# Kernel optimization log

Hardware: AMD Instinct MI355X
Metric: run time of the kernel (lower is better)

The kernel has to match this reference:

```python
import jax, jax.numpy as jnp
import numpy as np
import math

INPUT_SIZE = 1024
B, L1, L2 = 8, 2048, 2048


def setup_inputs() -> dict:
    key = jax.random.key(0)
    ks = jax.random.split(key, 10)
    s = 1.0 / math.sqrt(INPUT_SIZE)
    return {
        "Q": jax.random.normal(ks[0], (B, L1, INPUT_SIZE), dtype=jnp.float32),
        "K": jax.random.normal(ks[1], (B, L2, INPUT_SIZE), dtype=jnp.float32),
        "V": jax.random.normal(ks[2], (B, L2, INPUT_SIZE), dtype=jnp.float32),
        "K_mask": jax.random.randint(ks[3], (B, L2), 0, 2, dtype=jnp.int32),
        "Wq": jax.random.normal(ks[4], (INPUT_SIZE, INPUT_SIZE), dtype=jnp.float32) * s,
        "bq": jax.random.normal(ks[5], (INPUT_SIZE,), dtype=jnp.float32) * s,
        "Wk": jax.random.normal(ks[6], (INPUT_SIZE, INPUT_SIZE), dtype=jnp.float32) * s,
        "bk": jax.random.normal(ks[7], (INPUT_SIZE,), dtype=jnp.float32) * s,
        "Wv": jax.random.normal(ks[8], (INPUT_SIZE, INPUT_SIZE), dtype=jnp.float32) * s,
        "bv": jax.random.normal(ks[9], (INPUT_SIZE,), dtype=jnp.float32) * s,
    }


def reference(Q, K, V, K_mask, Wq, bq, Wk, bk, Wv, bv):
    # Linear projections (torch Linear: x @ W.T + b)
    q = jnp.einsum('bld,ed->ble', Q, Wq) + bq
    k = jnp.einsum('bld,ed->ble', K, Wk) + bk
    v = jnp.einsum('bld,ed->ble', V, Wv) + bv
    # scores: [B, L1, L2], scaled by sqrt(input_size)
    scores = jnp.einsum('bqd,bkd->bqk', q, k) / math.sqrt(INPUT_SIZE)
    # K_mask == 1 marks padding -> -inf before softmax
    scores = jnp.where(K_mask[:, None, :] == 1, -jnp.inf, scores)
    alpha = jax.nn.softmax(scores, axis=-1)
    matched_seq = jnp.einsum('bqk,bkd->bqd', alpha, v)
    return matched_seq
```

## Files before the change

### kernel.cpp

```cpp
#include <hip/hip_runtime.h>


using u16 = unsigned short;
using frag_ab = __attribute__((ext_vector_type(8))) short;
using frag_cd = __attribute__((ext_vector_type(4))) float;

#define BAR() asm volatile("s_barrier" ::: "memory")
#define WAITV(n) asm volatile("s_waitcnt vmcnt(" #n ")" ::: "memory")
#define WAITLGKM0() do { asm volatile("s_waitcnt lgkmcnt(0)" ::: "memory"); \
                         __builtin_amdgcn_sched_barrier(0); } while (0)
#define L(d, ab, h) (lds + (((d) * 4) + ((ab) * 2) + (h)) * 8192)

__device__ __forceinline__ u16 f2bf(float f) {
  union { float f; unsigned u; } c; c.f = f;
  unsigned u = c.u;
  return (u16)((u + 0x7FFFu + ((u >> 16) & 1u)) >> 16);
}
__device__ __forceinline__ u16 f2h(float f) {
  union { _Float16 h; u16 u; } c; c.h = (_Float16)f; return c.u;
}
__device__ __forceinline__ float h2f(u16 u) {
  union { u16 u; _Float16 h; } c; c.u = u; return (float)c.h;
}

__device__ __forceinline__ void async_ld16(const void* g, void* l) {
  __builtin_amdgcn_global_load_lds(
      (const __attribute__((address_space(1))) unsigned*)g,
      (__attribute__((address_space(3))) unsigned*)l, 16, 0, 0);
}

__global__ void cvtw3(const float* __restrict__ a, const float* __restrict__ b,
                      const float* __restrict__ c, u16* __restrict__ out) {
  const float* in = blockIdx.z == 0 ? a : (blockIdx.z == 1 ? b : c);
  u16* o = out + (long)blockIdx.z * 1048576L;
  long i = ((long)blockIdx.x * 256 + threadIdx.x) * 4;
  float4 v = *reinterpret_cast<const float4*>(in + i);
  *reinterpret_cast<ushort4*>(o + i) =
      make_ushort4(f2bf(v.x), f2bf(v.y), f2bf(v.z), f2bf(v.w));
}

__global__ void cvt3_f32_bf16(const float* __restrict__ q, const float* __restrict__ k,
                              const float* __restrict__ v, u16* __restrict__ out) {
  const float* in = blockIdx.z == 0 ? q : (blockIdx.z == 1 ? k : v);
  u16* o = out + (long)blockIdx.z * 16777216L;
  long i = ((long)blockIdx.x * 256 + threadIdx.x) * 4;
  float4 x = *reinterpret_cast<const float4*>(in + i);
  *reinterpret_cast<ushort4*>(o + i) =
      make_ushort4(f2bf(x.x), f2bf(x.y), f2bf(x.z), f2bf(x.w));
}

__device__ __forceinline__ void stage_half(const u16* __restrict__ g_rowbase,
                                           long Kstr, u16* l_half,
                                           int wave, int lane) {
  const int t = wave * 64 + lane;
  #pragma unroll
  for (int i = 0; i < 2; i++) {
    const int row = i * 64 + (t >> 3);
    const int cb  = (t & 7) * 16;
    const int cbs = cb ^ ((row & 7) << 4);
    async_ld16(g_rowbase + (long)row * Kstr + (cbs >> 1),
               l_half + i * 4096 + wave * 512);
  }
}

__device__ __forceinline__ frag_ab ld_frag(const u16* half_base, int r, int k) {
  const int idx = r * 64 + (k ^ ((r & 7) << 3));
  return *reinterpret_cast<const frag_ab*>(half_base + idx);
}

template<int OUT_MODE>
__device__ __forceinline__ void
gemm256_body(const u16* __restrict__ A, const u16* __restrict__ Bt,
             void* __restrict__ Cout, const float* __restrict__ bias,
             int M, int N, int K, long sA, long sB, long sC, float scale,
             u16* lds)
{
  const int gx = gridDim.x, gy = gridDim.y, gz = gridDim.z;
  const int nwg = gx * gy * gz;
  const int lin = ((int)blockIdx.z * gy + blockIdx.y) * gx + blockIdx.x;
  const int q8 = nwg >> 3, r8 = nwg & 7;
  const int xcd = lin & 7, idx8 = lin >> 3;
  const int swz = (xcd < r8 ? xcd * (q8 + 1) : r8 * (q8 + 1) + (xcd - r8) * q8) + idx8;
  const int z = swz / (gx * gy);
  const int rem = swz % (gx * gy);
  const int m0 = (rem / gx) * 256;
  const int n0 = (rem % gx) * 256;

  const u16* Ab = A + (long)z * sA;
  const u16* Bb = Bt + (long)z * sB;

  const int tid = threadIdx.x;
  const int wave = tid >> 6, lane = tid & 63;
  const int wm = wave >> 2, wn = wave & 3;
  const int ln15 = lane & 15, kof = (lane >> 4) * 8;
  const int rB0 = (wn & 1) * 64;
  const int NT = K >> 6;

  frag_cd acc[8][4];
  #pragma unroll
  for (int i = 0; i < 8; i++)
    #pragma unroll
    for (int j = 0; j < 4; j++)
      acc[i][j] = (frag_cd){0.f, 0.f, 0.f, 0.f};

  stage_half(Ab + (long)(m0 +   0) * K, K, L(0, 0, 0), wave, lane);
  stage_half(Ab + (long)(m0 + 128) * K, K, L(0, 0, 1), wave, lane);
  stage_half(Bb + (long)(n0 +   0) * K, K, L(0, 1, 0), wave, lane);
  stage_half(Bb + (long)(n0 + 128) * K, K, L(0, 1, 1), wave, lane);
  {
    const int t1 = (1 < NT) ? 1 : 0;
    stage_half(Bb + (long)(n0 +   0) * K + t1 * 64, K, L(1, 1, 0), wave, lane);
    stage_half(Bb + (long)(n0 + 128) * K + t1 * 64, K, L(1, 1, 1), wave, lane);
  }
  WAITV(4);
  BAR();

  for (int t = 0; t < NT; ++t) {
    const int d = t & 1;
    const u16* Al = L(d, 0, wm);
    const u16* Bl = L(d, 1, wn >> 1);
    const int tA = (t + 1 < NT) ? t + 1 : NT - 1;
    const int tB = (t + 2 < NT) ? t + 2 : NT - 1;

    frag_ab bf[4][2], af[2][2];

    #pragma unroll
    for (int bn = 0; bn < 4; ++bn)
      #pragma unroll
      for (int kk = 0; kk < 2; ++kk)
        bf[bn][kk] = ld_frag(Bl, rB0 + bn * 16 + ln15, kk * 32 + kof);
    #pragma unroll
    for (int am = 0; am < 2; ++am)
      #pragma unroll
      for (int kk = 0; kk < 2; ++kk)
        af[am][kk] = ld_frag(Al, am * 16 + ln15, kk * 32 + kof);
    stage_half(Ab + (long)(m0 +   0) * K + tA * 64, K, L(d ^ 1, 0, 0), wave, lane);
    stage_half(Ab + (long)(m0 + 128) * K + tA * 64, K, L(d ^ 1, 0, 1), wave, lane);
    BAR();
    __builtin_amdgcn_s_setprio(1);
    #pragma unroll
    for (int am = 0; am < 2; ++am)
      #pragma unroll
      for (int bn = 0; bn < 4; ++bn)
        #pragma unroll
        for (int kk = 0; kk < 2; ++kk)
          acc[am][bn] = __builtin_amdgcn_mfma_f32_16x16x32_bf16(af[am][kk], bf[bn][kk], acc[am][bn], 0, 0, 0);
    __builtin_amdgcn_s_setprio(0);
    BAR();

    #pragma unroll
    for (int am = 0; am < 2; ++am)
      #pragma unroll
      for (int kk = 0; kk < 2; ++kk)
        af[am][kk] = ld_frag(Al, (2 + am) * 16 + ln15, kk * 32 + kof);
    stage_half(Bb + (long)(n0 + 0) * K + tB * 64, K, L(d, 1, 0), wave, lane);
    BAR();
    __builtin_amdgcn_s_setprio(1);
    #pragma unroll
    for (int am = 0; am < 2; ++am)
      #pragma unroll
      for (int bn = 0; bn < 4; ++bn)
        #pragma unroll
        for (int kk = 0; kk < 2; ++kk)
          acc[2 + am][bn] = __builtin_amdgcn_mfma_f32_16x16x32_bf16(af[am][kk], bf[bn][kk], acc[2 + am][bn], 0, 0, 0);
    __builtin_amdgcn_s_setprio(0);
    BAR();

    #pragma unroll
    for (int am = 0; am < 2; ++am)
      #pragma unroll
      for (int kk = 0; kk < 2; ++kk)
        af[am][kk] = ld_frag(Al, (4 + am) * 16 + ln15, kk * 32 + kof);
    stage_half(Bb + (long)(n0 + 128) * K + tB * 64, K, L(d, 1, 1), wave, lane);
    BAR();
    __builtin_amdgcn_s_setprio(1);
    #pragma unroll
    for (int am = 0; am < 2; ++am)
      #pragma unroll
      for (int bn = 0; bn < 4; ++bn)
        #pragma unroll
        for (int kk = 0; kk < 2; ++kk)
          acc[4 + am][bn] = __builtin_amdgcn_mfma_f32_16x16x32_bf16(af[am][kk], bf[bn][kk], acc[4 + am][bn], 0, 0, 0);
    __builtin_amdgcn_s_setprio(0);
    BAR();

    #pragma unroll
    for (int am = 0; am < 2; ++am)
      #pragma unroll
      for (int kk = 0; kk < 2; ++kk)
        af[am][kk] = ld_frag(Al, (6 + am) * 16 + ln15, kk * 32 + kof);
    BAR();
    __builtin_amdgcn_s_setprio(1);
    #pragma unroll
    for (int am = 0; am < 2; ++am)
      #pragma unroll
      for (int bn = 0; bn < 4; ++bn)
        #pragma unroll
        for (int kk = 0; kk < 2; ++kk)
          acc[6 + am][bn] = __builtin_amdgcn_mfma_f32_16x16x32_bf16(af[am][kk], bf[bn][kk], acc[6 + am][bn], 0, 0, 0);
    __builtin_amdgcn_s_setprio(0);
    WAITV(4);
    BAR();
  }

  WAITV(0);
  BAR();

  const int cl = lane & 15;
  const int rb = (lane >> 4) * 4;

  if (OUT_MODE == 1 || OUT_MODE == 3) {
    u16* Wt = lds + wave * 8192;
    #pragma unroll
    for (int am = 0; am < 8; ++am)
      #pragma unroll
      for (int bn = 0; bn < 4; ++bn) {
        const int col = bn * 16 + cl;
        const float badd = bias ? bias[n0 + wn * 64 + col] : 0.f;
        #pragma unroll
        for (int r = 0; r < 4; ++r) {
          const int row = am * 16 + rb + r;
          const int slot = (col >> 3) ^ ((row >> 2) & 7);
          const float val = acc[am][bn][r] * scale + badd;
          Wt[row * 64 + slot * 8 + (col & 7)] = (OUT_MODE == 1) ? f2bf(val) : f2h(val);
        }
      }
    WAITLGKM0();
    u16* Cb = (u16*)Cout + (long)z * sC;
    #pragma unroll
    for (int i = 0; i < 16; ++i) {
      const int row = (lane >> 3) + i * 8;
      const int c = lane & 7;
      const int slot = c ^ ((row >> 2) & 7);
      frag_ab v = *reinterpret_cast<const frag_ab*>(Wt + row * 64 + slot * 8);
      const long grow = m0 + wm * 128 + row;
      const int gcol = n0 + wn * 64 + c * 8;
      *reinterpret_cast<frag_ab*>(Cb + grow * N + gcol) = v;
    }
  } else if (OUT_MODE == 0) {
    float* Wt = (float*)(void*)lds + wave * 4096;
    float* Cb = (float*)Cout + (long)z * sC;
    #pragma unroll
    for (int p = 0; p < 2; ++p) {
      #pragma unroll
      for (int am = 0; am < 8; ++am)
        #pragma unroll
        for (int bn = 0; bn < 2; ++bn) {
          const int col = bn * 16 + cl;
          #pragma unroll
          for (int r = 0; r < 4; ++r) {
            const int row = am * 16 + rb + r;
            const int slot = (col >> 2) ^ ((row >> 2) & 7);
            Wt[row * 32 + slot * 4 + (col & 3)] = acc[am][2 * p + bn][r] * scale;
          }
        }
      WAITLGKM0();
      #pragma unroll
      for (int i = 0; i < 16; ++i) {
        const int row = (lane >> 3) + i * 8;
        const int c = lane & 7;
        const int slot = c ^ ((row >> 2) & 7);
        float4 v = *reinterpret_cast<const float4*>(Wt + row * 32 + slot * 4);
        const long grow = m0 + wm * 128 + row;
        const int gcol = n0 + wn * 64 + p * 32 + c * 4;
        *reinterpret_cast<float4*>(Cb + grow * N + gcol) = v;
      }
      if (p == 0) WAITLGKM0();
    }
  } else {
    #pragma unroll
    for (int bn = 0; bn < 4; ++bn) {
      const int gcol = n0 + wn * 64 + bn * 16 + cl;
      const float badd = bias ? bias[gcol] : 0.f;
      #pragma unroll
      for (int am = 0; am < 8; ++am) {
        const int grow0 = m0 + wm * 128 + am * 16 + rb;
        ushort4 pk;
        pk.x = f2bf(acc[am][bn][0] * scale + badd);
        pk.y = f2bf(acc[am][bn][1] * scale + badd);
        pk.z = f2bf(acc[am][bn][2] * scale + badd);
        pk.w = f2bf(acc[am][bn][3] * scale + badd);
        const int bb = grow0 >> 11, l2 = grow0 & 2047;
        *reinterpret_cast<ushort4*>((u16*)Cout + ((long)bb * N + gcol) * 2048L + l2) = pk;
      }
    }
  }
}

__global__ void __launch_bounds__(512, 2)
proj_gemm(const u16* A, const u16* Bt, void* C, const float* bias,
          int M, int N, int K, long sA, long sB, long sC, float scale) {
  __shared__ u16 lds[8 * 8192];
  gemm256_body<1>(A, Bt, C, bias, M, N, K, sA, sB, sC, scale, lds);
}
__global__ void __launch_bounds__(512, 2)
projv_gemm(const u16* A, const u16* Bt, void* C, const float* bias,
           int M, int N, int K, long sA, long sB, long sC, float scale) {
  __shared__ u16 lds[8 * 8192];
  gemm256_body<2>(A, Bt, C, bias, M, N, K, sA, sB, sC, scale, lds);
}
__global__ void __launch_bounds__(512, 2)
qk_gemm(const u16* A, const u16* Bt, void* C, const float* bias,
        int M, int N, int K, long sA, long sB, long sC, float scale) {
  __shared__ u16 lds[8 * 8192];
  gemm256_body<3>(A, Bt, C, bias, M, N, K, sA, sB, sC, scale, lds);
}
__global__ void __launch_bounds__(512, 2)
pv_gemm(const u16* A, const u16* Bt, void* C, const float* bias,
        int M, int N, int K, long sA, long sB, long sC, float scale) {
  __shared__ u16 lds[8 * 8192];
  gemm256_body<0>(A, Bt, C, bias, M, N, K, sA, sB, sC, scale, lds);
}

__global__ void softmax_rows_h(const u16* __restrict__ S, const int* __restrict__ Km,
                               u16* __restrict__ P)
{
  const long row = blockIdx.x;
  const int b = (int)(row >> 11);
  const u16* s = S + row * 2048;
  const int* mask = Km + (long)b * 2048;
  u16* p = P + row * 2048;

  const int t = threadIdx.x;
  const int base = t * 8;

  ushort4 r0 = *reinterpret_cast<const ushort4*>(s + base);
  ushort4 r1 = *reinterpret_cast<const ushort4*>(s + base + 4);
  int4 mA = *reinterpret_cast<const int4*>(mask + base);
  int4 mB = *reinterpret_cast<const int4*>(mask + base + 4);

  float vals[8] = {h2f(r0.x), h2f(r0.y), h2f(r0.z), h2f(r0.w),
                   h2f(r1.x), h2f(r1.y), h2f(r1.z), h2f(r1.w)};
  const int mk[8] = {mA.x, mA.y, mA.z, mA.w, mB.x, mB.y, mB.z, mB.w};

  float mx = -3.0e38f;
  #pragma unroll
  for (int i = 0; i < 8; i++) if (!mk[i]) mx = fmaxf(mx, vals[i]);
  #pragma unroll
  for (int off = 32; off > 0; off >>= 1) mx = fmaxf(mx, __shfl_xor(mx, off));

  __shared__ float redm[4], reds[4];
  const int wave = t >> 6, lane = t & 63;
  if (lane == 0) redm[wave] = mx;
  __syncthreads();
  mx = fmaxf(fmaxf(redm[0], redm[1]), fmaxf(redm[2], redm[3]));

  float e[8]; float sum = 0.f;
  #pragma unroll
  for (int i = 0; i < 8; i++) { e[i] = mk[i] ? 0.f : __expf(vals[i] - mx); sum += e[i]; }
  #pragma unroll
  for (int off = 32; off > 0; off >>= 1) sum += __shfl_xor(sum, off);
  if (lane == 0) reds[wave] = sum;
  __syncthreads();
  sum = reds[0] + reds[1] + reds[2] + reds[3];
  const float inv = 1.f / sum;

  *reinterpret_cast<ushort4*>(p + base) =
      make_ushort4(f2bf(e[0]*inv), f2bf(e[1]*inv), f2bf(e[2]*inv), f2bf(e[3]*inv));
  *reinterpret_cast<ushort4*>(p + base + 4) =
      make_ushort4(f2bf(e[4]*inv), f2bf(e[5]*inv), f2bf(e[6]*inv), f2bf(e[7]*inv));
}

extern "C" void kernel_launch(void* const* d_in, const int* in_sizes, int n_in,
                              void* d_out, int out_size, void* d_ws, size_t ws_size,
                              hipStream_t stream) {
  (void)in_sizes; (void)n_in; (void)out_size;

  const float* Qin  = (const float*)d_in[0];
  const float* Kin  = (const float*)d_in[1];
  const float* Vin  = (const float*)d_in[2];
  const int*   Kmask = (const int*)d_in[3];
  const float* Wq = (const float*)d_in[4];
  const float* bq = (const float*)d_in[5];
  const float* Wk = (const float*)d_in[6];
  const float* bk = (const float*)d_in[7];
  const float* Wv = (const float*)d_in[8];
  const float* bv = (const float*)d_in[9];

  char* ws = (char*)d_ws;
  const size_t MB = 1024UL * 1024UL;
  const dim3 blk(256);
  const dim3 gblk(512);
  const float rs = 0.03125f;

  if (ws_size >= 226 * MB) {
    u16*  qb = (u16*)(ws);
    u16*  kb = (u16*)(ws + 32 * MB);
    u16*  vT = (u16*)(ws + 64 * MB);
    u16*  P  = (u16*)(ws + 96 * MB);
    u16*  Xq = (u16*)(ws + 96 * MB);
    u16*  S  = (u16*)(ws + 160 * MB);
    u16*  Wb = (u16*)(ws + 224 * MB);

    cvt3_f32_bf16<<<dim3(16384, 1, 3), blk, 0, stream>>>(Qin, Kin, Vin, Xq);
    cvtw3<<<dim3(1024, 1, 3), blk, 0, stream>>>(Wq, Wk, Wv, Wb);

    proj_gemm<<<dim3(4, 64, 1), gblk, 0, stream>>>(Xq, Wb, qb, bq,
        16384, 1024, 1024, 0, 0, 0, 1.f);
    proj_gemm<<<dim3(4, 64, 1), gblk, 0, stream>>>(Xq + 16777216L, Wb + 1048576L, kb, bk,
        16384, 1024, 1024, 0, 0, 0, 1.f);
    projv_gemm<<<dim3(4, 64, 1), gblk, 0, stream>>>(Xq + 2L * 16777216L, Wb + 2L * 1048576L, vT, bv,
        16384, 1024, 1024, 0, 0, 0, 1.f);

    qk_gemm<<<dim3(8, 8, 8), gblk, 0, stream>>>(qb, kb, S, nullptr,
        2048, 2048, 1024, 2048L * 1024, 2048L * 1024, 2048L * 2048, rs);
    softmax_rows_h<<<dim3(16384), blk, 0, stream>>>(S, Kmask, P);

    pv_gemm<<<dim3(4, 8, 8), gblk, 0, stream>>>(P, vT, d_out, nullptr,
        2048, 1024, 2048, 2048L * 2048, 1024L * 2048, 2048L * 1024, 1.f);
  } else if (ws_size >= 194 * MB) {
    u16*  qb = (u16*)(ws);
    u16*  kb = (u16*)(ws + 32 * MB);
    u16*  vT = (u16*)(ws + 64 * MB);
    u16*  P  = (u16*)(ws + 96 * MB);
    u16*  Xq = (u16*)(ws + 96 * MB);
    u16*  S  = (u16*)(ws + 160 * MB);
    u16*  Wb = (u16*)(ws + 186 * MB);

    cvt3_f32_bf16<<<dim3(16384, 1, 3), blk, 0, stream>>>(Qin, Kin, Vin, Xq);
    cvtw3<<<dim3(1024, 1, 3), blk, 0, stream>>>(Wq, Wk, Wv, Wb);

    proj_gemm<<<dim3(4, 64, 1), gblk, 0, stream>>>(Xq, Wb, qb, bq,
        16384, 1024, 1024, 0, 0, 0, 1.f);
    proj_gemm<<<dim3(4, 64, 1), gblk, 0, stream>>>(Xq + 16777216L, Wb + 1048576L, kb, bk,
        16384, 1024, 1024, 0, 0, 0, 1.f);
    projv_gemm<<<dim3(4, 64, 1), gblk, 0, stream>>>(Xq + 2L * 16777216L, Wb + 2L * 1048576L, vT, bv,
        16384, 1024, 1024, 0, 0, 0, 1.f);

    for (int h = 0; h < 2; h++) {
      const u16* qbH = qb + (long)(4 * h) * 2048 * 1024;
      const u16* kbH = kb + (long)(4 * h) * 2048 * 1024;
      qk_gemm<<<dim3(8, 8, 4), gblk, 0, stream>>>(qbH, kbH, S, nullptr,
          2048, 2048, 1024, 2048L * 1024, 2048L * 1024, 2048L * 2048, rs);
      softmax_rows_h<<<dim3(8192), blk, 0, stream>>>(
          S, Kmask + (long)(4 * h) * 2048, P + (long)(4 * h) * 2048 * 2048);
    }

    pv_gemm<<<dim3(4, 8, 8), gblk, 0, stream>>>(P, vT, d_out, nullptr,
        2048, 1024, 2048, 2048L * 2048, 1024L * 2048, 2048L * 1024, 1.f);
  } else {
    u16*  qb = (u16*)(ws);
    u16*  kb = (u16*)(ws + 32 * MB);
    u16*  vT = (u16*)(ws + 64 * MB);
    u16*  Xb = (u16*)(ws + 96 * MB);
    u16*  S  = (u16*)(ws + 96 * MB);
    u16*  P  = (u16*)(ws + 104 * MB);
    u16*  Wb = (u16*)(ws + 128 * MB);
    const long NQKV = 8L * 2048 * 1024;
    const long NW = 1024L * 1024;

    cvtw3<<<dim3(1024, 1, 3), blk, 0, stream>>>(Wq, Wk, Wv, Wb);
    cvt3_f32_bf16<<<dim3(16384, 1, 1), blk, 0, stream>>>(Qin, Qin, Qin, Xb);
    proj_gemm<<<dim3(4, 64, 1), gblk, 0, stream>>>(Xb, Wb, qb, bq,
        16384, 1024, 1024, 0, 0, 0, 1.f);
    cvt3_f32_bf16<<<dim3(16384, 1, 1), blk, 0, stream>>>(Kin, Kin, Kin, Xb);
    proj_gemm<<<dim3(4, 64, 1), gblk, 0, stream>>>(Xb, Wb + 1048576L, kb, bk,
        16384, 1024, 1024, 0, 0, 0, 1.f);
    cvt3_f32_bf16<<<dim3(16384, 1, 1), blk, 0, stream>>>(Vin, Vin, Vin, Xb);
    projv_gemm<<<dim3(4, 64, 1), gblk, 0, stream>>>(Xb, Wb + 2L * 1048576L, vT, bv,
        16384, 1024, 1024, 0, 0, 0, 1.f);
    (void)NQKV; (void)NW;

    for (int b = 0; b < 8; b++) {
      const u16* qbB = qb + (long)b * 2048 * 1024;
      const u16* kbB = kb + (long)b * 2048 * 1024;
      const u16* vTB = vT + (long)b * 1024 * 2048;
      float* outB = (float*)d_out + (long)b * 2048 * 1024;

      qk_gemm<<<dim3(8, 8, 1), gblk, 0, stream>>>(qbB, kbB, S, nullptr,
          2048, 2048, 1024, 0, 0, 0, rs);
      softmax_rows_h<<<dim3(2048), blk, 0, stream>>>(S, Kmask + (long)b * 2048, P);
      pv_gemm<<<dim3(4, 8, 1), gblk, 0, stream>>>(P, vTB, outB, nullptr,
          2048, 1024, 2048, 0, 0, 0, 1.f);
    }
  }
}
```

Measured before the change: 336.7 us.

## Merge QKV projections into one launch and rebalance GEMM prefetch staging

The three separate projection GEMM launches become a single 3-deep grid that selects weights, bias and output mode per z-slice, removing launch gaps and tail underutilization between projections. In the GEMM main loop the four global-to-LDS stage_half prefetches are now spread one per MFMA sub-phase instead of clustered, with an explicit lgkmcnt wait hint added. The template on output mode becomes a runtime argument, which may add branching or register pressure inside the shared core.

```diff
diff --git a/kernel.cpp b/kernel.cpp
--- a/kernel.cpp
+++ b/kernel.cpp
@@ -9,6 +9,7 @@
 #define WAITV(n) asm volatile("s_waitcnt vmcnt(" #n ")" ::: "memory")
 #define WAITLGKM0() do { asm volatile("s_waitcnt lgkmcnt(0)" ::: "memory"); \
                          __builtin_amdgcn_sched_barrier(0); } while (0)
+#define HINT_LGKM8() asm volatile("s_waitcnt lgkmcnt(8)" ::: "memory")
 #define L(d, ab, h) (lds + (((d) * 4) + ((ab) * 2) + (h)) * 8192)
 
 __device__ __forceinline__ u16 f2bf(float f) {
@@ -68,27 +69,27 @@
   return *reinterpret_cast<const frag_ab*>(half_base + idx);
 }
 
-template<int OUT_MODE>
-__device__ __forceinline__ void
-gemm256_body(const u16* __restrict__ A, const u16* __restrict__ Bt,
-             void* __restrict__ Cout, const float* __restrict__ bias,
-             int M, int N, int K, long sA, long sB, long sC, float scale,
-             u16* lds)
-{
+struct SwzOut { int z, m0, n0; };
+__device__ __forceinline__ SwzOut grid_swizzle() {
   const int gx = gridDim.x, gy = gridDim.y, gz = gridDim.z;
   const int nwg = gx * gy * gz;
   const int lin = ((int)blockIdx.z * gy + blockIdx.y) * gx + blockIdx.x;
   const int q8 = nwg >> 3, r8 = nwg & 7;
   const int xcd = lin & 7, idx8 = lin >> 3;
   const int swz = (xcd < r8 ? xcd * (q8 + 1) : r8 * (q8 + 1) + (xcd - r8) * q8) + idx8;
-  const int z = swz / (gx * gy);
+  SwzOut o;
+  o.z = swz / (gx * gy);
   const int rem = swz % (gx * gy);
-  const int m0 = (rem / gx) * 256;
-  const int n0 = (rem % gx) * 256;
-
-  const u16* Ab = A + (long)z * sA;
-  const u16* Bb = Bt + (long)z * sB;
-
+  o.m0 = (rem / gx) * 256;
+  o.n0 = (rem % gx) * 256;
+  return o;
+}
+
+__device__ __forceinline__ void
+gemm256_core(int out_mode, const u16* __restrict__ Ab, const u16* __restrict__ Bb,
+             void* __restrict__ Cb, const float* __restrict__ bias,
+             int N, int K, int m0, int n0, float scale, u16* lds)
+{
   const int tid = threadIdx.x;
   const int wave = tid >> 6, lane = tid & 63;
   const int wm = wave >> 2, wn = wave & 3;
@@ -134,8 +135,8 @@
       #pragma unroll
       for (int kk = 0; kk < 2; ++kk)
         af[am][kk] = ld_frag(Al, am * 16 + ln15, kk * 32 + kof);
-    stage_half(Ab + (long)(m0 +   0) * K + tA * 64, K, L(d ^ 1, 0, 0), wave, lane);
-    stage_half(Ab + (long)(m0 + 128) * K + tA * 64, K, L(d ^ 1, 0, 1), wave, lane);
+    stage_half(Ab + (long)(m0 + 0) * K + tA * 64, K, L(d ^ 1, 0, 0), wave, lane);
+    HINT_LGKM8();
     BAR();
     __builtin_amdgcn_s_setprio(1);
     #pragma unroll
@@ -153,7 +154,7 @@
       #pragma unroll
       for (int kk = 0; kk < 2; ++kk)
         af[am][kk] = ld_frag(Al, (2 + am) * 16 + ln15, kk * 32 + kof);
-    stage_half(Bb + (long)(n0 + 0) * K + tB * 64, K, L(d, 1, 0), wave, lane);
+    stage_half(Ab + (long)(m0 + 128) * K + tA * 64, K, L(d ^ 1, 0, 1), wave, lane);
     BAR();
     __builtin_amdgcn_s_setprio(1);
     #pragma unroll
@@ -171,7 +172,7 @@
       #pragma unroll
       for (int kk = 0; kk < 2; ++kk)
         af[am][kk] = ld_frag(Al, (4 + am) * 16 + ln15, kk * 32 + kof);
-    stage_half(Bb + (long)(n0 + 128) * K + tB * 64, K, L(d, 1, 1), wave, lane);
+    stage_half(Bb + (long)(n0 + 0) * K + tB * 64, K, L(d, 1, 0), wave, lane);
     BAR();
     __builtin_amdgcn_s_setprio(1);
     #pragma unroll
@@ -189,6 +190,7 @@
       #pragma unroll
       for (int kk = 0; kk < 2; ++kk)
         af[am][kk] = ld_frag(Al, (6 + am) * 16 + ln15, kk * 32 + kof);
+    stage_half(Bb + (long)(n0 + 128) * K + tB * 64, K, L(d, 1, 1), wave, lane);
     BAR();
     __builtin_amdgcn_s_setprio(1);
     #pragma unroll
@@ -209,7 +211,7 @@
   const int cl = lane & 15;
   const int rb = (lane >> 4) * 4;
 
-  if (OUT_MODE == 1 || OUT_MODE == 3) {
+  if (out_mode == 1 || out_mode == 3) {
     u16* Wt = lds + wave * 8192;
     #pragma unroll
     for (int am = 0; am < 8; ++am)
@@ -222,11 +224,11 @@
           const int row = am * 16 + rb + r;
           const int slot = (col >> 3) ^ ((row >> 2) & 7);
           const float val = acc[am][bn][r] * scale + badd;
-          Wt[row * 64 + slot * 8 + (col & 7)] = (OUT_MODE == 1) ? f2bf(val) : f2h(val);
+          Wt[row * 64 + slot * 8 + (col & 7)] = (out_mode == 1) ? f2bf(val) : f2h(val);
         }
       }
     WAITLGKM0();
-    u16* Cb = (u16*)Cout + (long)z * sC;
+    u16* Cp = (u16*)Cb;
     #pragma unroll
     for (int i = 0; i < 16; ++i) {
       const int row = (lane >> 3) + i * 8;
@@ -235,11 +237,11 @@
       frag_ab v = *reinterpret_cast<const frag_ab*>(Wt + row * 64 + slot * 8);
       const long grow = m0 + wm * 128 + row;
       const int gcol = n0 + wn * 64 + c * 8;
-      *reinterpret_cast<frag_ab*>(Cb + grow * N + gcol) = v;
+      *reinterpret_cast<frag_ab*>(Cp + grow * N + gcol) = v;
     }
-  } else if (OUT_MODE == 0) {
+  } else if (out_mode == 0) {
     float* Wt = (float*)(void*)lds + wave * 4096;
-    float* Cb = (float*)Cout + (long)z * sC;
+    float* Cp = (float*)Cb;
     #pragma unroll
     for (int p = 0; p < 2; ++p) {
       #pragma unroll
@@ -263,7 +265,7 @@
         float4 v = *reinterpret_cast<const float4*>(Wt + row * 32 + slot * 4);
         const long grow = m0 + wm * 128 + row;
         const int gcol = n0 + wn * 64 + p * 32 + c * 4;
-        *reinterpret_cast<float4*>(Cb + grow * N + gcol) = v;
+        *reinterpret_cast<float4*>(Cp + grow * N + gcol) = v;
       }
       if (p == 0) WAITLGKM0();
     }
@@ -281,35 +283,52 @@
         pk.z = f2bf(acc[am][bn][2] * scale + badd);
         pk.w = f2bf(acc[am][bn][3] * scale + badd);
         const int bb = grow0 >> 11, l2 = grow0 & 2047;
-        *reinterpret_cast<ushort4*>((u16*)Cout + ((long)bb * N + gcol) * 2048L + l2) = pk;
+        *reinterpret_cast<ushort4*>((u16*)Cb + ((long)bb * N + gcol) * 2048L + l2) = pk;
       }
     }
   }
 }
 
 __global__ void __launch_bounds__(512, 2)
-proj_gemm(const u16* A, const u16* Bt, void* C, const float* bias,
-          int M, int N, int K, long sA, long sB, long sC, float scale) {
+proj3_gemm(const u16* __restrict__ X, const u16* __restrict__ Wb,
+           const float* __restrict__ bq, const float* __restrict__ bk,
+           const float* __restrict__ bv, u16* __restrict__ qkb,
+           u16* __restrict__ vT)
+{
   __shared__ u16 lds[8 * 8192];
-  gemm256_body<1>(A, Bt, C, bias, M, N, K, sA, sB, sC, scale, lds);
-}
+  SwzOut s = grid_swizzle();
+  const u16* A = X + (long)s.z * 16777216L;
+  const u16* W = Wb + (long)s.z * 1048576L;
+  const float* bias = s.z == 0 ? bq : (s.z == 1 ? bk : bv);
+  if (s.z < 2)
+    gemm256_core(1, A, W, qkb + (long)s.z * 16777216L, bias,
+                 1024, 1024, s.m0, s.n0, 1.f, lds);
+  else
+    gemm256_core(2, A, W, vT, bias, 1024, 1024, s.m0, s.n0, 1.f, lds);
+}
+
 __global__ void __launch_bounds__(512, 2)
-projv_gemm(const u16* A, const u16* Bt, void* C, const float* bias,
-           int M, int N, int K, long sA, long sB, long sC, float scale) {
+proj1_gemm(int mode, const u16* A, const u16* W, void* C, const float* bias) {
   __shared__ u16 lds[8 * 8192];
-  gemm256_body<2>(A, Bt, C, bias, M, N, K, sA, sB, sC, scale, lds);
-}
+  SwzOut s = grid_swizzle();
+  gemm256_core(mode, A, W, C, bias, 1024, 1024, s.m0, s.n0, 1.f, lds);
+}
+
 __global__ void __launch_bounds__(512, 2)
-qk_gemm(const u16* A, const u16* Bt, void* C, const float* bias,
+qk_gemm(const u16* A, const u16* Bt, void* C,
         int M, int N, int K, long sA, long sB, long sC, float scale) {
   __shared__ u16 lds[8 * 8192];
-  gemm256_body<3>(A, Bt, C, bias, M, N, K, sA, sB, sC, scale, lds);
+  SwzOut s = grid_swizzle();
+  gemm256_core(3, A + (long)s.z * sA, Bt + (long)s.z * sB,
+               (u16*)C + (long)s.z * sC, nullptr, N, K, s.m0, s.n0, scale, lds);
 }
 __global__ void __launch_bounds__(512, 2)
-pv_gemm(const u16* A, const u16* Bt, void* C, const float* bias,
+pv_gemm(const u16* A, const u16* Bt, void* C,
         int M, int N, int K, long sA, long sB, long sC, float scale) {
   __shared__ u16 lds[8 * 8192];
-  gemm256_body<0>(A, Bt, C, bias, M, N, K, sA, sB, sC, scale, lds);
+  SwzOut s = grid_swizzle();
+  gemm256_core(0, A + (long)s.z * sA, Bt + (long)s.z * sB,
+               (float*)C + (long)s.z * sC, nullptr, N, K, s.m0, s.n0, scale, lds);
 }
 
 __global__ void softmax_rows_h(const u16* __restrict__ S, const int* __restrict__ Km,
@@ -385,7 +404,6 @@
 
   if (ws_size >= 226 * MB) {
     u16*  qb = (u16*)(ws);
-    u16*  kb = (u16*)(ws + 32 * MB);
     u16*  vT = (u16*)(ws + 64 * MB);
     u16*  P  = (u16*)(ws + 96 * MB);
     u16*  Xq = (u16*)(ws + 96 * MB);
@@ -395,22 +413,16 @@
     cvt3_f32_bf16<<<dim3(16384, 1, 3), blk, 0, stream>>>(Qin, Kin, Vin, Xq);
     cvtw3<<<dim3(1024, 1, 3), blk, 0, stream>>>(Wq, Wk, Wv, Wb);
 
-    proj_gemm<<<dim3(4, 64, 1), gblk, 0, stream>>>(Xq, Wb, qb, bq,
-        16384, 1024, 1024, 0, 0, 0, 1.f);
-    proj_gemm<<<dim3(4, 64, 1), gblk, 0, stream>>>(Xq + 16777216L, Wb + 1048576L, kb, bk,
-        16384, 1024, 1024, 0, 0, 0, 1.f);
-    projv_gemm<<<dim3(4, 64, 1), gblk, 0, stream>>>(Xq + 2L * 16777216L, Wb + 2L * 1048576L, vT, bv,
-        16384, 1024, 1024, 0, 0, 0, 1.f);
-
-    qk_gemm<<<dim3(8, 8, 8), gblk, 0, stream>>>(qb, kb, S, nullptr,
+    proj3_gemm<<<dim3(4, 64, 3), gblk, 0, stream>>>(Xq, Wb, bq, bk, bv, qb, vT);
+
+    qk_gemm<<<dim3(8, 8, 8), gblk, 0, stream>>>(qb, qb + 16777216L, S,
         2048, 2048, 1024, 2048L * 1024, 2048L * 1024, 2048L * 2048, rs);
     softmax_rows_h<<<dim3(16384), blk, 0, stream>>>(S, Kmask, P);
 
-    pv_gemm<<<dim3(4, 8, 8), gblk, 0, stream>>>(P, vT, d_out, nullptr,
+    pv_gemm<<<dim3(4, 8, 8), gblk, 0, stream>>>(P, vT, d_out,
         2048, 1024, 2048, 2048L * 2048, 1024L * 2048, 2048L * 1024, 1.f);
   } else if (ws_size >= 194 * MB) {
     u16*  qb = (u16*)(ws);
-    u16*  kb = (u16*)(ws + 32 * MB);
     u16*  vT = (u16*)(ws + 64 * MB);
     u16*  P  = (u16*)(ws + 96 * MB);
     u16*  Xq = (u16*)(ws + 96 * MB);
@@ -420,23 +432,18 @@
     cvt3_f32_bf16<<<dim3(16384, 1, 3), blk, 0, stream>>>(Qin, Kin, Vin, Xq);
     cvtw3<<<dim3(1024, 1, 3), blk, 0, stream>>>(Wq, Wk, Wv, Wb);
 
-    proj_gemm<<<dim3(4, 64, 1), gblk, 0, stream>>>(Xq, Wb, qb, bq,
-        16384, 1024, 1024, 0, 0, 0, 1.f);
-    proj_gemm<<<dim3(4, 64, 1), gblk, 0, stream>>>(Xq + 16777216L, Wb + 1048576L, kb, bk,
-        16384, 1024, 1024, 0, 0, 0, 1.f);
-    projv_gemm<<<dim3(4, 64, 1), gblk, 0, stream>>>(Xq + 2L * 16777216L, Wb + 2L * 1048576L, vT, bv,
-        16384, 1024, 1024, 0, 0, 0, 1.f);
+    proj3_gemm<<<dim3(4, 64, 3), gblk, 0, stream>>>(Xq, Wb, bq, bk, bv, qb, vT);
 
     for (int h = 0; h < 2; h++) {
       const u16* qbH = qb + (long)(4 * h) * 2048 * 1024;
-      const u16* kbH = kb + (long)(4 * h) * 2048 * 1024;
-      qk_gemm<<<dim3(8, 8, 4), gblk, 0, stream>>>(qbH, kbH, S, nullptr,
+      const u16* kbH = qb + 16777216L + (long)(4 * h) * 2048 * 1024;
+      qk_gemm<<<dim3(8, 8, 4), gblk, 0, stream>>>(qbH, kbH, S,
           2048, 2048, 1024, 2048L * 1024, 2048L * 1024, 2048L * 2048, rs);
       softmax_rows_h<<<dim3(8192), blk, 0, stream>>>(
           S, Kmask + (long)(4 * h) * 2048, P + (long)(4 * h) * 2048 * 2048);
     }
 
-    pv_gemm<<<dim3(4, 8, 8), gblk, 0, stream>>>(P, vT, d_out, nullptr,
+    pv_gemm<<<dim3(4, 8, 8), gblk, 0, stream>>>(P, vT, d_out,
         2048, 1024, 2048, 2048L * 2048, 1024L * 2048, 2048L * 1024, 1.f);
   } else {
     u16*  qb = (u16*)(ws);
@@ -446,20 +453,14 @@
     u16*  S  = (u16*)(ws + 96 * MB);
     u16*  P  = (u16*)(ws + 104 * MB);
     u16*  Wb = (u16*)(ws + 128 * MB);
-    const long NQKV = 8L * 2048 * 1024;
-    const long NW = 1024L * 1024;
 
     cvtw3<<<dim3(1024, 1, 3), blk, 0, stream>>>(Wq, Wk, Wv, Wb);
     cvt3_f32_bf16<<<dim3(16384, 1, 1), blk, 0, stream>>>(Qin, Qin, Qin, Xb);
-    proj_gemm<<<dim3(4, 64, 1), gblk, 0, stream>>>(Xb, Wb, qb, bq,
-        16384, 1024, 1024, 0, 0, 0, 1.f);
+    proj1_gemm<<<dim3(4, 64, 1), gblk, 0, stream>>>(1, Xb, Wb, qb, bq);
     cvt3_f32_bf16<<<dim3(16384, 1, 1), blk, 0, stream>>>(Kin, Kin, Kin, Xb);
-    proj_gemm<<<dim3(4, 64, 1), gblk, 0, stream>>>(Xb, Wb + 1048576L, kb, bk,
-        16384, 1024, 1024, 0, 0, 0, 1.f);
+    proj1_gemm<<<dim3(4, 64, 1), gblk, 0, stream>>>(1, Xb, Wb + 1048576L, kb, bk);
     cvt3_f32_bf16<<<dim3(16384, 1, 1), blk, 0, stream>>>(Vin, Vin, Vin, Xb);
-    projv_gemm<<<dim3(4, 64, 1), gblk, 0, stream>>>(Xb, Wb + 2L * 1048576L, vT, bv,
-        16384, 1024, 1024, 0, 0, 0, 1.f);
-    (void)NQKV; (void)NW;
+    proj1_gemm<<<dim3(4, 64, 1), gblk, 0, stream>>>(2, Xb, Wb + 2L * 1048576L, vT, bv);
 
     for (int b = 0; b < 8; b++) {
       const u16* qbB = qb + (long)b * 2048 * 1024;
@@ -467,10 +468,10 @@
       const u16* vTB = vT + (long)b * 1024 * 2048;
       float* outB = (float*)d_out + (long)b * 2048 * 1024;
 
-      qk_gemm<<<dim3(8, 8, 1), gblk, 0, stream>>>(qbB, kbB, S, nullptr,
+      qk_gemm<<<dim3(8, 8, 1), gblk, 0, stream>>>(qbB, kbB, S,
           2048, 2048, 1024, 0, 0, 0, rs);
       softmax_rows_h<<<dim3(2048), blk, 0, stream>>>(S, Kmask + (long)b * 2048, P);
-      pv_gemm<<<dim3(4, 8, 1), gblk, 0, stream>>>(P, vTB, outB, nullptr,
+      pv_gemm<<<dim3(4, 8, 1), gblk, 0, stream>>>(P, vTB, outB,
           2048, 1024, 2048, 0, 0, 0, 1.f);
     }
   }
```

Result: faster. 329.9 us, median of 2 (-2.0%).
